# Kernel tuning notes

Hardware: AMD Instinct MI355X
Metric: run time of the kernel (lower is better)

Reference implementation:

```python
import jax, jax.numpy as jnp
import numpy as np

D_MODEL = 1024
H = 16
D = D_MODEL // H  # 64 per head
D_FF = 4096
LN_EPS = 1e-5


def layer_norm(x, gamma, beta):
    mu = jnp.mean(x, axis=-1, keepdims=True)
    var = jnp.mean(jnp.square(x - mu), axis=-1, keepdims=True)
    return (x - mu) * jax.lax.rsqrt(var + LN_EPS) * gamma + beta


def setup_inputs() -> dict:
    key = jax.random.key(0)
    ks = jax.random.split(key, 12)
    s = 1.0 / np.sqrt(D_MODEL)
    sf = 1.0 / np.sqrt(D_FF)
    return {
        "x": jax.random.normal(ks[0], (2, 2048, D_MODEL), jnp.float32),
        "src_mask": 0,
        "w_q": jax.random.normal(ks[1], (D_MODEL, D_MODEL), jnp.float32) * s,
        "w_k": jax.random.normal(ks[2], (D_MODEL, D_MODEL), jnp.float32) * s,
        "w_v": jax.random.normal(ks[3], (D_MODEL, D_MODEL), jnp.float32) * s,
        "w_0": jax.random.normal(ks[4], (D_MODEL, D_MODEL), jnp.float32) * s,
        "b_0": jnp.zeros((D_MODEL,), jnp.float32),
        "w_1": jax.random.normal(ks[5], (D_MODEL, D_FF), jnp.float32) * s,
        "b_1": jnp.zeros((D_FF,), jnp.float32),
        "w_2": jax.random.normal(ks[6], (D_FF, D_MODEL), jnp.float32) * sf,
        "b_2": jnp.zeros((D_MODEL,), jnp.float32),
        "g_1": jnp.ones((D_MODEL,), jnp.float32),
        "be_1": jnp.zeros((D_MODEL,), jnp.float32),
        "g_2": jnp.ones((D_MODEL,), jnp.float32),
        "be_2": jnp.zeros((D_MODEL,), jnp.float32),
    }


def reference(x, src_mask, w_q, w_k, w_v, w_0, b_0, w_1, b_1, w_2, b_2, g_1, be_1, g_2, be_2):
    N, S, _ = x.shape
    # --- pre-LN self-attention branch ---
    x_n = layer_norm(x, g_1, be_1)
    q = (x_n @ w_q).reshape(N, S, H, D).transpose(0, 2, 1, 3)  # [N,H,S,D]
    k = (x_n @ w_k).reshape(N, S, H, D).transpose(0, 2, 1, 3)
    v = (x_n @ w_v).reshape(N, S, H, D).transpose(0, 2, 1, 3)
    scores = jnp.einsum('nhqd,nhkd->nhqk', q, k) / np.sqrt(D)
    # src_mask == 0 (falsy) in the original -> no masking applied
    attn = jax.nn.softmax(scores, axis=-1)
    out = jnp.einsum('nhqk,nhkd->nhqd', attn, v)
    out = out.transpose(0, 2, 1, 3).reshape(N, S, H * D)
    attn_out = out @ w_0 + b_0
    x = x + attn_out  # dropout is identity in eval
    # --- pre-LN feedforward branch ---
    x_n = layer_norm(x, g_2, be_2)
    ff = jax.nn.relu(x_n @ w_1 + b_1) @ w_2 + b_2
    return x + ff
```

## Files before the change

kernel.cpp:

```cpp
#include <hip/hip_runtime.h>

typedef __bf16 bf16x8 __attribute__((ext_vector_type(8)));
typedef float f32x4 __attribute__((ext_vector_type(4)));
typedef unsigned short u16x8 __attribute__((ext_vector_type(8)));
typedef unsigned short u16x4 __attribute__((ext_vector_type(4)));

__device__ __forceinline__ unsigned short f2bf_bits(float f) {
  unsigned u = __float_as_uint(f);
  return (unsigned short)((u + 0x7FFFu + ((u >> 16) & 1u)) >> 16);
}

__device__ __forceinline__ float exp2_amd(float x) {
  return __builtin_amdgcn_exp2f(x);
}

__device__ __forceinline__ unsigned cvt_pk_bf16(float a, float b) {
  unsigned r;
  asm("v_cvt_pk_bf16_f32 %0, %1, %2" : "=v"(r) : "v"(a), "v"(b));
  return r;
}

__device__ __forceinline__ float red16_max(float x) {
  unsigned a = __float_as_uint(x), b = a;
  asm("v_permlane16_swap_b32 %0, %1" : "+v"(a), "+v"(b));
  return fmaxf(__uint_as_float(a), __uint_as_float(b));
}
__device__ __forceinline__ float red32_max(float x) {
  unsigned a = __float_as_uint(x), b = a;
  asm("v_permlane32_swap_b32 %0, %1" : "+v"(a), "+v"(b));
  return fmaxf(__uint_as_float(a), __uint_as_float(b));
}
__device__ __forceinline__ float red16_sum(float x) {
  unsigned a = __float_as_uint(x), b = a;
  asm("v_permlane16_swap_b32 %0, %1" : "+v"(a), "+v"(b));
  return __uint_as_float(a) + __uint_as_float(b);
}
__device__ __forceinline__ float red32_sum(float x) {
  unsigned a = __float_as_uint(x), b = a;
  asm("v_permlane32_swap_b32 %0, %1" : "+v"(a), "+v"(b));
  return __uint_as_float(a) + __uint_as_float(b);
}

__device__ __forceinline__ void gload16(const void* g, void* l) {
  __builtin_amdgcn_global_load_lds(
      (const __attribute__((address_space(1))) unsigned int*)g,
      (__attribute__((address_space(3))) unsigned int*)l, 16, 0, 0);
}

__global__ __launch_bounds__(256) void prep_k(
    const float* __restrict__ s0, const float* __restrict__ s1,
    const float* __restrict__ s2, const float* __restrict__ s3,
    const float* __restrict__ s4, const float* __restrict__ s5,
    unsigned short* __restrict__ d0, unsigned short* __restrict__ d1,
    unsigned short* __restrict__ d2, unsigned short* __restrict__ d3,
    unsigned short* __restrict__ d4, unsigned short* __restrict__ d5,
    const float* __restrict__ x, const float* __restrict__ g1,
    const float* __restrict__ be1, unsigned short* __restrict__ xn) {
  const int t = blockIdx.x;
  const int tid = threadIdx.x;
  if (t >= 12288) {
    const int row = t - 12288;
    const float4 v = ((const float4*)(x + (size_t)row * 1024))[tid];
    float s = v.x + v.y + v.z + v.w;
    float s2 = v.x * v.x + v.y * v.y + v.z * v.z + v.w * v.w;
#pragma unroll
    for (int m = 1; m < 64; m <<= 1) {
      s += __shfl_xor(s, m);
      s2 += __shfl_xor(s2, m);
    }
    __shared__ float red[8];
    const int w = tid >> 6;
    if ((tid & 63) == 0) { red[w] = s; red[4 + w] = s2; }
    __syncthreads();
    s = red[0] + red[1] + red[2] + red[3];
    s2 = red[4] + red[5] + red[6] + red[7];
    const float mu = s * (1.f / 1024.f);
    const float rs_ = rsqrtf(s2 * (1.f / 1024.f) - mu * mu + 1e-5f);
    const float4 gg = ((const float4*)g1)[tid];
    const float4 bb = ((const float4*)be1)[tid];
    u16x4 pack;
    pack.x = f2bf_bits((v.x - mu) * rs_ * gg.x + bb.x);
    pack.y = f2bf_bits((v.y - mu) * rs_ * gg.y + bb.y);
    pack.z = f2bf_bits((v.z - mu) * rs_ * gg.z + bb.z);
    pack.w = f2bf_bits((v.w - mu) * rs_ * gg.w + bb.w);
    *(u16x4*)(xn + (size_t)row * 1024 + tid * 4) = pack;
    return;
  }
  const float* src;
  unsigned short* dst;
  int R, C, bx, by;
  if (t < 4096) {
    const int i = t >> 10, id = t & 1023;
    src = i == 0 ? s0 : i == 1 ? s1 : i == 2 ? s2 : s3;
    dst = i == 0 ? d0 : i == 1 ? d1 : i == 2 ? d2 : d3;
    R = 1024; C = 1024; bx = id & 31; by = id >> 5;
  } else if (t < 8192) {
    const int id = t - 4096;
    src = s4; dst = d4; R = 1024; C = 4096; bx = id & 127; by = id >> 7;
  } else {
    const int id = t - 8192;
    src = s5; dst = d5; R = 4096; C = 1024; bx = id & 31; by = id >> 5;
  }
  __shared__ float tile[32][33];
  const int tx = tid & 31, ty = tid >> 5;
  const size_t c0 = (size_t)bx * 32, r0 = (size_t)by * 32;
#pragma unroll
  for (int i = 0; i < 4; i++)
    tile[ty + i * 8][tx] = src[(r0 + ty + i * 8) * C + c0 + tx];
  __syncthreads();
#pragma unroll
  for (int i = 0; i < 4; i++) {
    int c = ty + i * 8;
    dst[(c0 + c) * R + r0 + tx] = f2bf_bits(tile[tx][c]);
  }
}

__global__ __launch_bounds__(256) void w0red_ln(const float* __restrict__ p,
                                                const float* __restrict__ b0,
                                                const float* __restrict__ x,
                                                const float* __restrict__ g,
                                                const float* __restrict__ be,
                                                float* __restrict__ x1f,
                                                unsigned short* __restrict__ xn) {
  const int row = blockIdx.x, tid = threadIdx.x;
  const size_t base = (size_t)row * 1024 + tid * 4;
  const float4 xv = *(const float4*)(x + base);
  const float4 bb0 = ((const float4*)b0)[tid];
  const float4 p0 = *(const float4*)(p + base);
  const float4 p1 = *(const float4*)(p + 4194304 + base);
  float4 v;
  v.x = xv.x + bb0.x + p0.x + p1.x;
  v.y = xv.y + bb0.y + p0.y + p1.y;
  v.z = xv.z + bb0.z + p0.z + p1.z;
  v.w = xv.w + bb0.w + p0.w + p1.w;
  *(float4*)(x1f + base) = v;
  float s = v.x + v.y + v.z + v.w;
  float s2 = v.x * v.x + v.y * v.y + v.z * v.z + v.w * v.w;
#pragma unroll
  for (int m = 1; m < 64; m <<= 1) {
    s += __shfl_xor(s, m);
    s2 += __shfl_xor(s2, m);
  }
  __shared__ float red[8];
  const int w = tid >> 6;
  if ((tid & 63) == 0) { red[w] = s; red[4 + w] = s2; }
  __syncthreads();
  s = red[0] + red[1] + red[2] + red[3];
  s2 = red[4] + red[5] + red[6] + red[7];
  const float mu = s * (1.f / 1024.f);
  const float rs_ = rsqrtf(s2 * (1.f / 1024.f) - mu * mu + 1e-5f);
  const float4 gg = ((const float4*)g)[tid];
  const float4 bb = ((const float4*)be)[tid];
  u16x4 pack;
  pack.x = f2bf_bits((v.x - mu) * rs_ * gg.x + bb.x);
  pack.y = f2bf_bits((v.y - mu) * rs_ * gg.y + bb.y);
  pack.z = f2bf_bits((v.z - mu) * rs_ * gg.z + bb.z);
  pack.w = f2bf_bits((v.w - mu) * rs_ * gg.w + bb.w);
  *(u16x4*)(xn + base) = pack;
}

__global__ __launch_bounds__(256) void ff2red(const float* __restrict__ p,
                                              const float* __restrict__ bias,
                                              const float* __restrict__ res,
                                              float* __restrict__ out) {
  const size_t i = ((size_t)blockIdx.x * 256 + threadIdx.x) * 8;
  const int col = (int)(i & 1023);
  const float4 b0 = *(const float4*)(bias + col);
  const float4 b1 = *(const float4*)(bias + col + 4);
  const float4 r0 = *(const float4*)(res + i);
  const float4 r1 = *(const float4*)(res + i + 4);
  const float4 p00 = *(const float4*)(p + i);
  const float4 p01 = *(const float4*)(p + i + 4);
  const float4 p10 = *(const float4*)(p + 4194304 + i);
  const float4 p11 = *(const float4*)(p + 4194304 + i + 4);
  float4 o0 = {b0.x + r0.x + p00.x + p10.x, b0.y + r0.y + p00.y + p10.y,
               b0.z + r0.z + p00.z + p10.z, b0.w + r0.w + p00.w + p10.w};
  float4 o1 = {b1.x + r1.x + p01.x + p11.x, b1.y + r1.y + p01.y + p11.y,
               b1.z + r1.z + p01.z + p11.z, b1.w + r1.w + p01.w + p11.w};
  *(float4*)(out + i) = o0;
  *(float4*)(out + i + 4) = o1;
}

template <int EPI>
__global__ __launch_bounds__(256) void gemm_bt(
    const unsigned short* __restrict__ A, const unsigned short* __restrict__ Bt,
    const float* __restrict__ bias, const float* __restrict__ res,
    void* __restrict__ Cv, int M, int N, int K, int KL) {
  __shared__ __align__(16) unsigned short As[2][128 * 64];
  __shared__ __align__(16) unsigned short Bs[2][128 * 64];
  const int tid = threadIdx.x, lane = tid & 63, w = tid >> 6;
  const int lo = lane & 15, hi = lane >> 4;
  const int l8 = lane >> 3, l7 = lane & 7;
  const int scol = ((l7 ^ l8) << 3);
  const int nwg = gridDim.x * gridDim.y;
  int bid = blockIdx.y * gridDim.x + blockIdx.x;
  if ((nwg & 7) == 0) bid = (bid & 7) * (nwg >> 3) + (bid >> 3);
  const int bx = bid % gridDim.x, by = bid / gridDim.x;
  const size_t rowBase = (size_t)by * 128;
  const size_t colBase = (size_t)bx * 128;
  const int kOff = blockIdx.z * KL;
  f32x4 acc[4][4];
#pragma unroll
  for (int i = 0; i < 4; i++)
#pragma unroll
    for (int j = 0; j < 4; j++) acc[i][j] = (f32x4){0.f, 0.f, 0.f, 0.f};
  const int wr = (w >> 1) * 64, wc = (w & 1) * 64;
  const unsigned short* aSrc = A + (rowBase + (size_t)w * 32 + l8) * K + scol + kOff;
  const unsigned short* bSrc = Bt + (colBase + (size_t)w * 32 + l8) * K + scol + kOff;

  const int NT = KL >> 6;
  auto stage = [&](int t, int buf) {
    const int kb = t << 6;
#pragma unroll
    for (int c = 0; c < 4; c++) {
      gload16(aSrc + (size_t)c * 8 * K + kb, &As[buf][(w * 4 + c) * 512]);
      gload16(bSrc + (size_t)c * 8 * K + kb, &Bs[buf][(w * 4 + c) * 512]);
    }
  };

  stage(0, 0);
  stage(1, 1);
  asm volatile("s_waitcnt vmcnt(8)" ::: "memory");
  __builtin_amdgcn_s_barrier();

  for (int t = 0; t < NT; ++t) {
    const int cur = t & 1;
    const char* asb = (const char*)As[cur];
    const char* bsb = (const char*)Bs[cur];
    __builtin_amdgcn_s_setprio(1);
#pragma unroll
    for (int ks = 0; ks < 2; ks++) {
      bf16x8 af[4], bfr[4];
      const int kbyte = ks * 64 + (hi << 4);
#pragma unroll
      for (int i = 0; i < 4; i++) {
        const int ar = wr + i * 16 + lo;
        af[i] = *(const bf16x8*)(asb + ar * 128 + (kbyte ^ ((ar & 7) << 4)));
        const int br = wc + i * 16 + lo;
        bfr[i] = *(const bf16x8*)(bsb + br * 128 + (kbyte ^ ((br & 7) << 4)));
      }
#pragma unroll
      for (int i = 0; i < 4; i++)
#pragma unroll
        for (int j = 0; j < 4; j++)
          acc[i][j] = __builtin_amdgcn_mfma_f32_16x16x32_bf16(af[i], bfr[j], acc[i][j], 0, 0, 0);
    }
    __builtin_amdgcn_s_setprio(0);
    asm volatile("s_waitcnt lgkmcnt(0)" ::: "memory");
    __builtin_amdgcn_s_barrier();
    if (t + 2 < NT) {
      stage(t + 2, cur);
      asm volatile("s_waitcnt vmcnt(8)" ::: "memory");
    } else {
      asm volatile("s_waitcnt vmcnt(0)" ::: "memory");
    }
    __builtin_amdgcn_s_barrier();
  }

  const size_t zOff = (size_t)blockIdx.z * M * N;
#pragma unroll
  for (int i = 0; i < 4; i++) {
#pragma unroll
    for (int r = 0; r < 4; r++) {
      const size_t row = rowBase + wr + i * 16 + hi * 4 + r;
#pragma unroll
      for (int j = 0; j < 4; j++) {
        const size_t col = colBase + wc + j * 16 + lo;
        float v = acc[i][j][r];
        if (EPI == 2) {
          ((unsigned short*)Cv)[row * N + col] = f2bf_bits(fmaxf(v + bias[col], 0.f));
        } else if (EPI == 3) {
          ((float*)Cv)[zOff + row * N + col] = v;
        } else {
          ((unsigned short*)Cv)[row * N + col] = f2bf_bits(v);
        }
      }
    }
  }
}

__global__ __launch_bounds__(256) void attn_k(const unsigned short* __restrict__ Q,
                                              const unsigned short* __restrict__ K,
                                              const unsigned short* __restrict__ V,
                                              unsigned short* __restrict__ O) {
  __shared__ __align__(16) unsigned short Ks[2][128 * 64];
  __shared__ __align__(16) unsigned short Vt[2][64 * 128];
  const int tid = threadIdx.x, lane = tid & 63, w = tid >> 6;
  const int lo = lane & 15, hi = lane >> 4;
  const int l8 = lane >> 3, l7 = lane & 7;
  const int scol = ((l7 ^ l8) << 3);
  const int b = blockIdx.x;
  const int qt = b >> 5;
  const int hn = (b & 7) + 8 * ((b >> 3) & 3);
  const int h = hn & 15, n = hn >> 4;
  const size_t tRow0 = (size_t)n * 2048;
  const int colBase = h * 64;
  const int LD = 3072;
  const float SC = 0.125f * 1.44269504f;

  const unsigned short* qrowA = Q + (tRow0 + qt * 128 + w * 32 + lo) * LD + colBase;
  const unsigned short* qrowB = qrowA + 16 * LD;
  const bf16x8 qf[2][2] = {
      {*(const bf16x8*)(qrowA + hi * 8), *(const bf16x8*)(qrowA + 32 + hi * 8)},
      {*(const bf16x8*)(qrowB + hi * 8), *(const bf16x8*)(qrowB + 32 + hi * 8)}};
  float m2[2] = {-1e30f, -1e30f}, l_r[2] = {0.f, 0.f};
  f32x4 oacc[2][4];
#pragma unroll
  for (int g = 0; g < 2; g++)
#pragma unroll
    for (int d = 0; d < 4; d++) oacc[g][d] = (f32x4){0.f, 0.f, 0.f, 0.f};

  const int vkv = tid & 127, vdg = tid >> 7;
  const unsigned short* vbase = V + (tRow0 + vkv) * LD + colBase + vdg * 32;
  const unsigned short* kbase = K + (tRow0 + (size_t)w * 32 + l8) * LD + colBase + scol;

  auto vwrite = [&](char* vt, u16x8 a0, u16x8 a1, u16x8 a2, u16x8 a3) {
#pragma unroll
    for (int j = 0; j < 8; j++) {
      const int d0 = vdg * 32 + j;
      const int sw = ((vkv * 2) ^ (j << 4));
      *(unsigned short*)(vt + d0 * 256 + sw) = a0[j];
      *(unsigned short*)(vt + (d0 + 8) * 256 + sw) = a1[j];
      *(unsigned short*)(vt + (d0 + 16) * 256 + sw) = a2[j];
      *(unsigned short*)(vt + (d0 + 24) * 256 + sw) = a3[j];
    }
  };

  u16x8 v0 = *(const u16x8*)(vbase);
  u16x8 v1 = *(const u16x8*)(vbase + 8);
  u16x8 v2 = *(const u16x8*)(vbase + 16);
  u16x8 v3 = *(const u16x8*)(vbase + 24);
#pragma unroll
  for (int c = 0; c < 4; c++)
    gload16(kbase + (size_t)c * 8 * LD, &Ks[0][(w * 4 + c) * 512]);
  vwrite((char*)Vt[0], v0, v1, v2, v3);
  __syncthreads();

  for (int t = 0; t < 16; ++t) {
    const int cur = t & 1;
    if (t < 15) {
      const unsigned short* vs = vbase + (size_t)(t + 1) * 128 * LD;
      v0 = *(const u16x8*)(vs);
      v1 = *(const u16x8*)(vs + 8);
      v2 = *(const u16x8*)(vs + 16);
      v3 = *(const u16x8*)(vs + 24);
#pragma unroll
      for (int c = 0; c < 4; c++)
        gload16(kbase + ((size_t)(t + 1) * 128 + c * 8) * LD, &Ks[cur ^ 1][(w * 4 + c) * 512]);
    }
    f32x4 s[2][8];
    const char* ksb = (const char*)Ks[cur];
    __builtin_amdgcn_s_setprio(1);
#pragma unroll
    for (int f = 0; f < 8; f++) {
      const int kr = f * 16 + lo;
      const bf16x8 b0 = *(const bf16x8*)(ksb + kr * 128 + ((hi * 16) ^ ((kr & 7) << 4)));
      const bf16x8 b1 = *(const bf16x8*)(ksb + kr * 128 + ((64 + hi * 16) ^ ((kr & 7) << 4)));
#pragma unroll
      for (int g = 0; g < 2; g++) {
        s[g][f] = __builtin_amdgcn_mfma_f32_16x16x32_bf16(b0, qf[g][0], (f32x4){0.f, 0.f, 0.f, 0.f}, 0, 0, 0);
        s[g][f] = __builtin_amdgcn_mfma_f32_16x16x32_bf16(b1, qf[g][1], s[g][f], 0, 0, 0);
      }
    }
    __builtin_amdgcn_s_setprio(0);
    unsigned W2[2][8][2];
#pragma unroll
    for (int g = 0; g < 2; g++) {
      float mx = -1e30f;
#pragma unroll
      for (int f = 0; f < 8; f++)
        mx = fmaxf(mx, fmaxf(fmaxf(s[g][f][0], s[g][f][1]), fmaxf(s[g][f][2], s[g][f][3])));
      mx = red16_max(mx);
      mx = red32_max(mx);
      const float mx2v = mx * SC;
      if (__any(mx2v > m2[g] + 8.f)) {
        const float mn = fmaxf(m2[g], mx2v);
        const float al = exp2_amd(m2[g] - mn);
        l_r[g] *= al;
        m2[g] = mn;
#pragma unroll
        for (int r = 0; r < 4; r++) {
          const float alr = __shfl(al, hi * 4 + r);
#pragma unroll
          for (int d = 0; d < 4; d++) oacc[g][d][r] *= alr;
        }
      }
      float lsum = 0.f;
#pragma unroll
      for (int f = 0; f < 8; f++) {
        float p0 = exp2_amd(fmaf(s[g][f][0], SC, -m2[g]));
        float p1 = exp2_amd(fmaf(s[g][f][1], SC, -m2[g]));
        float p2 = exp2_amd(fmaf(s[g][f][2], SC, -m2[g]));
        float p3 = exp2_amd(fmaf(s[g][f][3], SC, -m2[g]));
        lsum += (p0 + p1) + (p2 + p3);
        W2[g][f][0] = cvt_pk_bf16(p0, p1);
        W2[g][f][1] = cvt_pk_bf16(p2, p3);
      }
      l_r[g] += lsum;
    }
    __builtin_amdgcn_s_setprio(1);
#pragma unroll
    for (int ks = 0; ks < 4; ks++) {
      union { unsigned u[4]; bf16x8 v; } apu[2];
#pragma unroll
      for (int g = 0; g < 2; g++) {
        unsigned wa[2], wb[2];
#pragma unroll
        for (int hh = 0; hh < 2; hh++) {
          unsigned X = W2[g][ks * 2][hh], Y = W2[g][ks * 2 + 1][hh];
          asm("v_permlane32_swap_b32 %0, %1" : "+v"(X), "+v"(Y));
          const unsigned Bx = __shfl_xor((int)Y, 16);
          const unsigned Ax = __shfl_xor((int)X, 16);
          wa[hh] = (hi & 1) ? Bx : X;
          wb[hh] = (hi & 1) ? Y : Ax;
        }
        apu[g].u[0] = wa[0]; apu[g].u[1] = wa[1]; apu[g].u[2] = wb[0]; apu[g].u[3] = wb[1];
      }
      const int kbyte = ks * 64 + (hi << 4);
#pragma unroll
      for (int d = 0; d < 4; d++) {
        const int dr = d * 16 + lo;
        const bf16x8 bv = *(const bf16x8*)((const char*)Vt[cur] + dr * 256 + (kbyte ^ ((dr & 7) << 4)));
        oacc[0][d] = __builtin_amdgcn_mfma_f32_16x16x32_bf16(apu[0].v, bv, oacc[0][d], 0, 0, 0);
        oacc[1][d] = __builtin_amdgcn_mfma_f32_16x16x32_bf16(apu[1].v, bv, oacc[1][d], 0, 0, 0);
      }
    }
    __builtin_amdgcn_s_setprio(0);
    if (t < 15) vwrite((char*)Vt[cur ^ 1], v0, v1, v2, v3);
    __syncthreads();
  }
#pragma unroll
  for (int g = 0; g < 2; g++) {
    const float l = red32_sum(red16_sum(l_r[g]));
    const float inv = 1.f / l;
#pragma unroll
    for (int r = 0; r < 4; r++) {
      const float invr = __shfl(inv, hi * 4 + r);
      const size_t row = tRow0 + qt * 128 + w * 32 + g * 16 + hi * 4 + r;
#pragma unroll
      for (int d = 0; d < 4; d++)
        O[row * 1024 + colBase + d * 16 + lo] = f2bf_bits(oacc[g][d][r] * invr);
    }
  }
}

extern "C" void kernel_launch(void* const* d_in, const int* in_sizes, int n_in,
                              void* d_out, int out_size, void* d_ws, size_t ws_size,
                              hipStream_t stream) {
  (void)in_sizes; (void)n_in; (void)out_size; (void)ws_size;
  const float* x   = (const float*)d_in[0];
  const float* w_q = (const float*)d_in[2];
  const float* w_k = (const float*)d_in[3];
  const float* w_v = (const float*)d_in[4];
  const float* w_0 = (const float*)d_in[5];
  const float* b_0 = (const float*)d_in[6];
  const float* w_1 = (const float*)d_in[7];
  const float* b_1 = (const float*)d_in[8];
  const float* w_2 = (const float*)d_in[9];
  const float* b_2 = (const float*)d_in[10];
  const float* g_1 = (const float*)d_in[11];
  const float* be_1 = (const float*)d_in[12];
  const float* g_2 = (const float*)d_in[13];
  const float* be_2 = (const float*)d_in[14];

  char* ws = (char*)d_ws;
  size_t off = 0;
  auto alloc = [&](size_t bytes) {
    void* p = ws + off;
    off += (bytes + 255) & ~(size_t)255;
    return p;
  };
  const size_t MB = 1024 * 1024;
  unsigned short* wt_q = (unsigned short*)alloc(2 * MB);
  unsigned short* wt_k = (unsigned short*)alloc(2 * MB);
  unsigned short* wt_v = (unsigned short*)alloc(2 * MB);
  unsigned short* wt_0 = (unsigned short*)alloc(2 * MB);
  unsigned short* wt_1 = (unsigned short*)alloc(8 * MB);
  unsigned short* wt_2 = (unsigned short*)alloc(8 * MB);
  unsigned short* xn   = (unsigned short*)alloc(8 * MB);
  unsigned short* qkv  = (unsigned short*)alloc(24 * MB);
  unsigned short* aO   = (unsigned short*)alloc(8 * MB);
  float*          x1f  = (float*)alloc(16 * MB);
  unsigned short* ff1  = (unsigned short*)alloc(32 * MB);
  float* w0part  = (float*)ff1;
  float* ff2part = (float*)qkv;

  prep_k<<<16384, 256, 0, stream>>>(w_q, w_k, w_v, w_0, w_1, w_2,
                                    wt_q, wt_k, wt_v, wt_0, wt_1, wt_2,
                                    x, g_1, be_1, xn);
  gemm_bt<0><<<dim3(24, 32), 256, 0, stream>>>(xn, wt_q, nullptr, nullptr, qkv, 4096, 3072, 1024, 1024);
  attn_k<<<512, 256, 0, stream>>>(qkv, qkv + 1024, qkv + 2048, aO);
  gemm_bt<3><<<dim3(8, 32, 2), 256, 0, stream>>>(aO, wt_0, nullptr, nullptr, w0part, 4096, 1024, 1024, 512);
  w0red_ln<<<4096, 256, 0, stream>>>(w0part, b_0, x, g_2, be_2, x1f, xn);
  gemm_bt<2><<<dim3(32, 32), 256, 0, stream>>>(xn, wt_1, b_1, nullptr, ff1, 4096, 4096, 1024, 1024);
  gemm_bt<3><<<dim3(8, 32, 2), 256, 0, stream>>>(ff1, wt_2, nullptr, nullptr, ff2part, 4096, 1024, 4096, 2048);
  ff2red<<<2048, 256, 0, stream>>>(ff2part, b_2, x1f, (float*)d_out);
}
```

Before: 249.1 us.

## Split attention block across 8 waves with 16 query rows each

The attention kernel now launches 512 threads (8 waves) per block instead of 256. Each wave handles 16 query rows instead of 32, so its score, softmax and PV accumulator state is halved. K/V tile loading is spread over twice as many threads, with fewer loads per thread. The aim is more waves in flight and lower register pressure per wave to hide latency. The cost is that each K/V fragment read from LDS now feeds fewer MFMAs, so LDS traffic per FLOP doubles, and barriers span more waves.

After: 244.3 us, median of 2. No clear change (-1.9%).

```diff
diff --git a/kernel.cpp b/kernel.cpp
--- a/kernel.cpp
+++ b/kernel.cpp
@@ -279,7 +279,7 @@
   }
 }
 
-__global__ __launch_bounds__(256) void attn_k(const unsigned short* __restrict__ Q,
+__global__ __launch_bounds__(512) void attn_k(const unsigned short* __restrict__ Q,
                                               const unsigned short* __restrict__ K,
                                               const unsigned short* __restrict__ V,
                                               unsigned short* __restrict__ O) {
@@ -298,42 +298,34 @@
   const int LD = 3072;
   const float SC = 0.125f * 1.44269504f;
 
-  const unsigned short* qrowA = Q + (tRow0 + qt * 128 + w * 32 + lo) * LD + colBase;
-  const unsigned short* qrowB = qrowA + 16 * LD;
-  const bf16x8 qf[2][2] = {
-      {*(const bf16x8*)(qrowA + hi * 8), *(const bf16x8*)(qrowA + 32 + hi * 8)},
-      {*(const bf16x8*)(qrowB + hi * 8), *(const bf16x8*)(qrowB + 32 + hi * 8)}};
-  float m2[2] = {-1e30f, -1e30f}, l_r[2] = {0.f, 0.f};
-  f32x4 oacc[2][4];
-#pragma unroll
-  for (int g = 0; g < 2; g++)
-#pragma unroll
-    for (int d = 0; d < 4; d++) oacc[g][d] = (f32x4){0.f, 0.f, 0.f, 0.f};
+  const unsigned short* qrow = Q + (tRow0 + qt * 128 + w * 16 + lo) * LD + colBase;
+  const bf16x8 qf0 = *(const bf16x8*)(qrow + hi * 8);
+  const bf16x8 qf1 = *(const bf16x8*)(qrow + 32 + hi * 8);
+  float m2 = -1e30f, l_r = 0.f;
+  f32x4 oacc[4];
+#pragma unroll
+  for (int d = 0; d < 4; d++) oacc[d] = (f32x4){0.f, 0.f, 0.f, 0.f};
 
   const int vkv = tid & 127, vdg = tid >> 7;
-  const unsigned short* vbase = V + (tRow0 + vkv) * LD + colBase + vdg * 32;
-  const unsigned short* kbase = K + (tRow0 + (size_t)w * 32 + l8) * LD + colBase + scol;
-
-  auto vwrite = [&](char* vt, u16x8 a0, u16x8 a1, u16x8 a2, u16x8 a3) {
+  const unsigned short* vbase = V + (tRow0 + vkv) * LD + colBase + vdg * 16;
+  const unsigned short* kbase = K + (tRow0 + (size_t)w * 16 + l8) * LD + colBase + scol;
+
+  auto vwrite = [&](char* vt, u16x8 a0, u16x8 a1) {
 #pragma unroll
     for (int j = 0; j < 8; j++) {
-      const int d0 = vdg * 32 + j;
+      const int d0 = vdg * 16 + j;
       const int sw = ((vkv * 2) ^ (j << 4));
       *(unsigned short*)(vt + d0 * 256 + sw) = a0[j];
       *(unsigned short*)(vt + (d0 + 8) * 256 + sw) = a1[j];
-      *(unsigned short*)(vt + (d0 + 16) * 256 + sw) = a2[j];
-      *(unsigned short*)(vt + (d0 + 24) * 256 + sw) = a3[j];
     }
   };
 
   u16x8 v0 = *(const u16x8*)(vbase);
   u16x8 v1 = *(const u16x8*)(vbase + 8);
-  u16x8 v2 = *(const u16x8*)(vbase + 16);
-  u16x8 v3 = *(const u16x8*)(vbase + 24);
-#pragma unroll
-  for (int c = 0; c < 4; c++)
-    gload16(kbase + (size_t)c * 8 * LD, &Ks[0][(w * 4 + c) * 512]);
-  vwrite((char*)Vt[0], v0, v1, v2, v3);
+#pragma unroll
+  for (int c = 0; c < 2; c++)
+    gload16(kbase + (size_t)c * 8 * LD, &Ks[0][(w * 2 + c) * 512]);
+  vwrite((char*)Vt[0], v0, v1);
   __syncthreads();
 
   for (int t = 0; t < 16; ++t) {
@@ -342,13 +334,11 @@
       const unsigned short* vs = vbase + (size_t)(t + 1) * 128 * LD;
       v0 = *(const u16x8*)(vs);
       v1 = *(const u16x8*)(vs + 8);
-      v2 = *(const u16x8*)(vs + 16);
-      v3 = *(const u16x8*)(vs + 24);
-#pragma unroll
-      for (int c = 0; c < 4; c++)
-        gload16(kbase + ((size_t)(t + 1) * 128 + c * 8) * LD, &Ks[cur ^ 1][(w * 4 + c) * 512]);
-    }
-    f32x4 s[2][8];
+#pragma unroll
+      for (int c = 0; c < 2; c++)
+        gload16(kbase + ((size_t)(t + 1) * 128 + c * 8) * LD, &Ks[cur ^ 1][(w * 2 + c) * 512]);
+    }
+    f32x4 s[8];
     const char* ksb = (const char*)Ks[cur];
     __builtin_amdgcn_s_setprio(1);
 #pragma unroll
@@ -356,90 +346,79 @@
       const int kr = f * 16 + lo;
       const bf16x8 b0 = *(const bf16x8*)(ksb + kr * 128 + ((hi * 16) ^ ((kr & 7) << 4)));
       const bf16x8 b1 = *(const bf16x8*)(ksb + kr * 128 + ((64 + hi * 16) ^ ((kr & 7) << 4)));
-#pragma unroll
-      for (int g = 0; g < 2; g++) {
-        s[g][f] = __builtin_amdgcn_mfma_f32_16x16x32_bf16(b0, qf[g][0], (f32x4){0.f, 0.f, 0.f, 0.f}, 0, 0, 0);
-        s[g][f] = __builtin_amdgcn_mfma_f32_16x16x32_bf16(b1, qf[g][1], s[g][f], 0, 0, 0);
+      s[f] = __builtin_amdgcn_mfma_f32_16x16x32_bf16(b0, qf0, (f32x4){0.f, 0.f, 0.f, 0.f}, 0, 0, 0);
+      s[f] = __builtin_amdgcn_mfma_f32_16x16x32_bf16(b1, qf1, s[f], 0, 0, 0);
+    }
+    __builtin_amdgcn_s_setprio(0);
+    float mx = -1e30f;
+#pragma unroll
+    for (int f = 0; f < 8; f++)
+      mx = fmaxf(mx, fmaxf(fmaxf(s[f][0], s[f][1]), fmaxf(s[f][2], s[f][3])));
+    mx = red16_max(mx);
+    mx = red32_max(mx);
+    const float mx2v = mx * SC;
+    if (__any(mx2v > m2 + 8.f)) {
+      const float mn = fmaxf(m2, mx2v);
+      const float al = exp2_amd(m2 - mn);
+      l_r *= al;
+      m2 = mn;
+#pragma unroll
+      for (int r = 0; r < 4; r++) {
+        const float alr = __shfl(al, hi * 4 + r);
+#pragma unroll
+        for (int d = 0; d < 4; d++) oacc[d][r] *= alr;
       }
     }
-    __builtin_amdgcn_s_setprio(0);
-    unsigned W2[2][8][2];
-#pragma unroll
-    for (int g = 0; g < 2; g++) {
-      float mx = -1e30f;
-#pragma unroll
-      for (int f = 0; f < 8; f++)
-        mx = fmaxf(mx, fmaxf(fmaxf(s[g][f][0], s[g][f][1]), fmaxf(s[g][f][2], s[g][f][3])));
-      mx = red16_max(mx);
-      mx = red32_max(mx);
-      const float mx2v = mx * SC;
-      if (__any(mx2v > m2[g] + 8.f)) {
-        const float mn = fmaxf(m2[g], mx2v);
-        const float al = exp2_amd(m2[g] - mn);
-        l_r[g] *= al;
-        m2[g] = mn;
-#pragma unroll
-        for (int r = 0; r < 4; r++) {
-          const float alr = __shfl(al, hi * 4 + r);
-#pragma unroll
-          for (int d = 0; d < 4; d++) oacc[g][d][r] *= alr;
-        }
+    unsigned W2[8][2];
+    float lsum = 0.f;
+#pragma unroll
+    for (int f = 0; f < 8; f++) {
+      float p0 = exp2_amd(fmaf(s[f][0], SC, -m2));
+      float p1 = exp2_amd(fmaf(s[f][1], SC, -m2));
+      float p2 = exp2_amd(fmaf(s[f][2], SC, -m2));
+      float p3 = exp2_amd(fmaf(s[f][3], SC, -m2));
+      lsum += (p0 + p1) + (p2 + p3);
+      W2[f][0] = cvt_pk_bf16(p0, p1);
+      W2[f][1] = cvt_pk_bf16(p2, p3);
+    }
+    l_r += lsum;
+    __builtin_amdgcn_s_setprio(1);
+#pragma unroll
+    for (int ks = 0; ks < 4; ks++) {
+      unsigned wa[2], wb[2];
+#pragma unroll
+      for (int hh = 0; hh < 2; hh++) {
+        unsigned X = W2[ks * 2][hh], Y = W2[ks * 2 + 1][hh];
+        asm("v_permlane32_swap_b32 %0, %1" : "+v"(X), "+v"(Y));
+        const unsigned Bx = __shfl_xor((int)Y, 16);
+        const unsigned Ax = __shfl_xor((int)X, 16);
+        wa[hh] = (hi & 1) ? Bx : X;
+        wb[hh] = (hi & 1) ? Y : Ax;
       }
-      float lsum = 0.f;
-#pragma unroll
-      for (int f = 0; f < 8; f++) {
-        float p0 = exp2_amd(fmaf(s[g][f][0], SC, -m2[g]));
-        float p1 = exp2_amd(fmaf(s[g][f][1], SC, -m2[g]));
-        float p2 = exp2_amd(fmaf(s[g][f][2], SC, -m2[g]));
-        float p3 = exp2_amd(fmaf(s[g][f][3], SC, -m2[g]));
-        lsum += (p0 + p1) + (p2 + p3);
-        W2[g][f][0] = cvt_pk_bf16(p0, p1);
-        W2[g][f][1] = cvt_pk_bf16(p2, p3);
-      }
-      l_r[g] += lsum;
-    }
-    __builtin_amdgcn_s_setprio(1);
-#pragma unroll
-    for (int ks = 0; ks < 4; ks++) {
-      union { unsigned u[4]; bf16x8 v; } apu[2];
-#pragma unroll
-      for (int g = 0; g < 2; g++) {
-        unsigned wa[2], wb[2];
-#pragma unroll
-        for (int hh = 0; hh < 2; hh++) {
-          unsigned X = W2[g][ks * 2][hh], Y = W2[g][ks * 2 + 1][hh];
-          asm("v_permlane32_swap_b32 %0, %1" : "+v"(X), "+v"(Y));
-          const unsigned Bx = __shfl_xor((int)Y, 16);
-          const unsigned Ax = __shfl_xor((int)X, 16);
-          wa[hh] = (hi & 1) ? Bx : X;
-          wb[hh] = (hi & 1) ? Y : Ax;
-        }
-        apu[g].u[0] = wa[0]; apu[g].u[1] = wa[1]; apu[g].u[2] = wb[0]; apu[g].u[3] = wb[1];
-      }
+      union { unsigned u[4]; bf16x8 v; } apu;
+      apu.u[0] = wa[0]; apu.u[1] = wa[1]; apu.u[2] = wb[0]; apu.u[3] = wb[1];
       const int kbyte = ks * 64 + (hi << 4);
 #pragma unroll
       for (int d = 0; d < 4; d++) {
         const int dr = d * 16 + lo;
         const bf16x8 bv = *(const bf16x8*)((const char*)Vt[cur] + dr * 256 + (kbyte ^ ((dr & 7) << 4)));
-        oacc[0][d] = __builtin_amdgcn_mfma_f32_16x16x32_bf16(apu[0].v, bv, oacc[0][d], 0, 0, 0);
-        oacc[1][d] = __builtin_amdgcn_mfma_f32_16x16x32_bf16(apu[1].v, bv, oacc[1][d], 0, 0, 0);
+        oacc[d] = __builtin_amdgcn_mfma_f32_16x16x32_bf16(apu.v, bv, oacc[d], 0, 0, 0);
       }
     }
     __builtin_amdgcn_s_setprio(0);
-    if (t < 15) vwrite((char*)Vt[cur ^ 1], v0, v1, v2, v3);
+    if (t < 15) vwrite((char*)Vt[cur ^ 1], v0, v1);
     __syncthreads();
   }
-#pragma unroll
-  for (int g = 0; g < 2; g++) {
-    const float l = red32_sum(red16_sum(l_r[g]));
+  {
+    const float l = red32_sum(red16_sum(l_r));
     const float inv = 1.f / l;
 #pragma unroll
     for (int r = 0; r < 4; r++) {
       const float invr = __shfl(inv, hi * 4 + r);
-      const size_t row = tRow0 + qt * 128 + w * 32 + g * 16 + hi * 4 + r;
+      const size_t row = tRow0 + qt * 128 + w * 16 + hi * 4 + r;
 #pragma unroll
       for (int d = 0; d < 4; d++)
-        O[row * 1024 + colBase + d * 16 + lo] = f2bf_bits(oacc[g][d][r] * invr);
+        O[row * 1024 + colBase + d * 16 + lo] = f2bf_bits(oacc[d][r] * invr);
     }
   }
 }
@@ -489,7 +468,7 @@
                                     wt_q, wt_k, wt_v, wt_0, wt_1, wt_2,
                                     x, g_1, be_1, xn);
   gemm_bt<0><<<dim3(24, 32), 256, 0, stream>>>(xn, wt_q, nullptr, nullptr, qkv, 4096, 3072, 1024, 1024);
-  attn_k<<<512, 256, 0, stream>>>(qkv, qkv + 1024, qkv + 2048, aO);
+  attn_k<<<512, 512, 0, stream>>>(qkv, qkv + 1024, qkv + 2048, aO);
   gemm_bt<3><<<dim3(8, 32, 2), 256, 0, stream>>>(aO, wt_0, nullptr, nullptr, w0part, 4096, 1024, 1024, 512);
   w0red_ln<<<4096, 256, 0, stream>>>(w0part, b_0, x, g_2, be_2, x1f, xn);
   gemm_bt<2><<<dim3(32, 32), 256, 0, stream>>>(xn, wt_1, b_1, nullptr, ff1, 4096, 4096, 1024, 1024);
```
